# Performance work log

Measured on AMD Instinct MI355X. Metric: run time of the kernel, lower is better.

## Reference

```python
import jax, jax.numpy as jnp
import numpy as np

# dims
B, N, D, H, L = 2, 4096, 768, 12, 2
DH = D // H          # 64, equals BigBird block_size
BS = 64              # block size
NB = N // BS         # 64 blocks
R = 3                # num_random_blocks
FF = 4 * D
EPS = 1e-12          # BigBird layer_norm_eps


def _ln(x, g, b):
    mu = jnp.mean(x, -1, keepdims=True)
    var = jnp.mean(jnp.square(x - mu), -1, keepdims=True)
    return (x - mu) * jax.lax.rsqrt(var + EPS) * g + b


def _gelu_new(x):
    c = np.sqrt(2.0 / np.pi).astype(np.float32)
    return 0.5 * x * (1.0 + jnp.tanh(c * (x + 0.044715 * x * x * x)))


def _block_sparse_attn(q, k, v, rb):
    # q,k,v: [B,H,N,DH]; rb: [H,NB,R] random block ids (constant)
    scale = 1.0 / np.sqrt(DH).astype(np.float32)
    qb = q.reshape(B, H, NB, BS, DH)
    kb = k.reshape(B, H, NB, BS, DH)
    vb = v.reshape(B, H, NB, BS, DH)
    M = NB - 2
    mids = jnp.arange(1, NB - 1)
    win = jnp.stack([mids - 1, mids, mids + 1], -1)                    # [M,3]
    glb = jnp.broadcast_to(jnp.array([0, NB - 1], jnp.int32), (M, 2))  # [M,2]
    idx = jnp.concatenate([
        jnp.broadcast_to(glb[None], (H, M, 2)),
        jnp.broadcast_to(win[None], (H, M, 3)),
        rb[:, 1:NB - 1, :]], axis=-1)                                  # [H,M,8]
    hh = jnp.arange(H)[:, None, None]
    # gather key/value blocks: [B,H,M,8,BS,DH] -> [B,H,M,512,DH]
    kg = kb[:, hh, idx].reshape(B, H, M, -1, DH)
    vg = vb[:, hh, idx].reshape(B, H, M, -1, DH)
    qm = qb[:, :, 1:NB - 1]                                            # [B,H,M,BS,DH]
    s = jnp.einsum('bhmqd,bhmkd->bhmqk', qm, kg) * scale
    cm = jnp.einsum('bhmqk,bhmkd->bhmqd', jax.nn.softmax(s, -1), vg)
    # first and last query blocks attend globally (full attention)
    qe = jnp.stack([qb[:, :, 0], qb[:, :, -1]], 2)                     # [B,H,2,BS,DH]
    se = jnp.einsum('bheqd,bhkd->bheqk', qe, k) * scale
    ce = jnp.einsum('bheqk,bhkd->bheqd', jax.nn.softmax(se, -1), v)
    out = jnp.concatenate([ce[:, :, :1], cm, ce[:, :, 1:]], axis=2)    # [B,H,NB,BS,DH]
    return out.reshape(B, H, N, DH)


def _forward(inputs_embeds, rand_blocks, pos_emb, tt_emb, emb_ln_g, emb_ln_b,
             Wq, bq, Wk, bk, Wv, bv, Wo, bo, ln1_g, ln1_b,
             Wi, bi, Wd, bd, ln2_g, ln2_b, fc_w, fc_b):
    x = inputs_embeds + pos_emb[None] + tt_emb                         # embeddings (token_type id 0)
    x = _ln(x, emb_ln_g, emb_ln_b)
    for l in range(L):
        q = (x @ Wq[l] + bq[l]).reshape(B, N, H, DH).transpose(0, 2, 1, 3)
        k = (x @ Wk[l] + bk[l]).reshape(B, N, H, DH).transpose(0, 2, 1, 3)
        v = (x @ Wv[l] + bv[l]).reshape(B, N, H, DH).transpose(0, 2, 1, 3)
        ctx = _block_sparse_attn(q, k, v, rand_blocks[l])
        ctx = ctx.transpose(0, 2, 1, 3).reshape(B, N, D)
        a = _ln(x + ctx @ Wo[l] + bo[l], ln1_g[l], ln1_b[l])
        h = _gelu_new(a @ Wi[l] + bi[l])
        x = _ln(a + h @ Wd[l] + bd[l], ln2_g[l], ln2_b[l])
    pooled = jnp.mean(x, axis=1)                                       # [B,D]; dropout is identity at eval
    return (pooled @ fc_w + fc_b).squeeze()                            # [B]


def setup_inputs() -> dict:
    key = jax.random.key(0)
    ks = jax.random.split(key, 24)
    s = 0.02
    nrm = lambda k, shp: jax.random.normal(k, shp, jnp.float32) * s
    return {
        'inputs_embeds': jax.random.normal(ks[0], (B, N, D), jnp.float32),
        'rand_blocks': jax.random.randint(ks[1], (L, H, NB, R), 0, NB, jnp.int32),
        'pos_emb': nrm(ks[2], (N, D)),
        'tt_emb': nrm(ks[3], (D,)),
        'emb_ln_g': jnp.ones((D,), jnp.float32), 'emb_ln_b': jnp.zeros((D,), jnp.float32),
        'Wq': nrm(ks[4], (L, D, D)), 'bq': jnp.zeros((L, D), jnp.float32),
        'Wk': nrm(ks[5], (L, D, D)), 'bk': jnp.zeros((L, D), jnp.float32),
        'Wv': nrm(ks[6], (L, D, D)), 'bv': jnp.zeros((L, D), jnp.float32),
        'Wo': nrm(ks[7], (L, D, D)), 'bo': jnp.zeros((L, D), jnp.float32),
        'ln1_g': jnp.ones((L, D), jnp.float32), 'ln1_b': jnp.zeros((L, D), jnp.float32),
        'Wi': nrm(ks[8], (L, D, FF)), 'bi': jnp.zeros((L, FF), jnp.float32),
        'Wd': nrm(ks[9], (L, FF, D)), 'bd': jnp.zeros((L, D), jnp.float32),
        'ln2_g': jnp.ones((L, D), jnp.float32), 'ln2_b': jnp.zeros((L, D), jnp.float32),
        'fc_w': nrm(ks[10], (D, 1)), 'fc_b': jnp.zeros((1,), jnp.float32),
    }


def reference(inputs_embeds, rand_blocks, pos_emb, tt_emb, emb_ln_g, emb_ln_b,
              Wq, bq, Wk, bk, Wv, bv, Wo, bo, ln1_g, ln1_b,
              Wi, bi, Wd, bd, ln2_g, ln2_b, fc_w, fc_b):
    return _forward(inputs_embeds, rand_blocks, pos_emb, tt_emb, emb_ln_g, emb_ln_b,
                    Wq, bq, Wk, bk, Wv, bv, Wo, bo, ln1_g, ln1_b,
                    Wi, bi, Wd, bd, ln2_g, ln2_b, fc_w, fc_b)
```

## Files before the change

kernel.cpp:

```cpp
#include <hip/hip_runtime.h>
#include <math.h>

#define B_ 2
#define N_ 4096
#define D_ 768
#define H_ 12
#define DH_ 64
#define NB_ 64
#define FF_ 3072
#define LAYERS_ 2
#define ROWS_ (B_ * N_)

typedef __attribute__((ext_vector_type(8))) short s16x8;
typedef __attribute__((ext_vector_type(8))) unsigned short u16x8;
typedef __attribute__((ext_vector_type(4))) float f32x4;

typedef const __attribute__((address_space(1))) unsigned int ga_u32;
typedef __attribute__((address_space(3))) unsigned int lds_u32;

static __device__ __forceinline__ float gelu_fast(float x) {
    float z2 = 1.5957691216057308f * x * (1.0f + 0.044715f * x * x);
    return x * __builtin_amdgcn_rcpf(1.0f + __expf(-z2));
}

static __device__ __forceinline__ unsigned bf16_rne(float f) {
    unsigned u = __float_as_uint(f);
    return (u + 0x7FFFu + ((u >> 16) & 1u)) >> 16;
}
static __device__ __forceinline__ float bfh2f(unsigned short h) {
    return __uint_as_float(((unsigned)h) << 16);
}

__global__ __launch_bounds__(256)
void prep_weights(const float* __restrict__ Wq, const float* __restrict__ Wk,
                  const float* __restrict__ Wv, const float* __restrict__ Wo,
                  const float* __restrict__ Wi, const float* __restrict__ Wd,
                  unsigned short* __restrict__ Wt) {
    const size_t LW = 7077888;
    int bid = blockIdx.x;
    int l = bid / 1728, r = bid % 1728;
    const float* W; unsigned short* T; int K, N, t, nx;
    if (r < 576) {
        int which = r / 144; t = r % 144; nx = 12; K = 768; N = 768;
        W = (which == 0 ? Wq : which == 1 ? Wk : which == 2 ? Wv : Wo) + (size_t)l * D_ * D_;
        T = Wt + l * LW + (size_t)(which < 3 ? which * 768 * 768 : 2304 * 768);
    } else if (r < 1152) {
        t = r - 576; nx = 48; K = 768; N = 3072;
        W = Wi + (size_t)l * D_ * FF_;
        T = Wt + l * LW + (size_t)(2304 * 768 + 768 * 768);
    } else {
        t = r - 1152; nx = 12; K = 3072; N = 768;
        W = Wd + (size_t)l * FF_ * D_;
        T = Wt + l * LW + (size_t)(2304 * 768 + 768 * 768 + 3072 * 768);
    }
    const int bx = t % nx, by = t / nx;
    __shared__ unsigned short tile[64][72];
    const int k0 = by * 64, n0 = bx * 64;
    const int tt = threadIdx.x;
    const int rr = tt >> 2, c0 = (tt & 3) * 16;
    const float* src = W + (size_t)(k0 + rr) * N + n0 + c0;
#pragma unroll
    for (int j = 0; j < 4; ++j) {
        float4 v = *(const float4*)(src + j * 4);
        tile[rr][c0 + j * 4 + 0] = (unsigned short)bf16_rne(v.x);
        tile[rr][c0 + j * 4 + 1] = (unsigned short)bf16_rne(v.y);
        tile[rr][c0 + j * 4 + 2] = (unsigned short)bf16_rne(v.z);
        tile[rr][c0 + j * 4 + 3] = (unsigned short)bf16_rne(v.w);
    }
    __syncthreads();
    const int nr = tt >> 2, kc = (tt & 3) * 16;
    unsigned short* dst = T + (size_t)(n0 + nr) * K + k0 + kc;
    ushort4 o;
#pragma unroll
    for (int j = 0; j < 4; ++j) {
        o.x = tile[kc + j * 4 + 0][nr];
        o.y = tile[kc + j * 4 + 1][nr];
        o.z = tile[kc + j * 4 + 2][nr];
        o.w = tile[kc + j * 4 + 3][nr];
        *(ushort4*)(dst + j * 4) = o;
    }
}

template <int OMODE>
__global__ __launch_bounds__(256)
void gemm_bt(const unsigned short* __restrict__ A, const unsigned short* __restrict__ Bt,
             const float* __restrict__ bias, void* __restrict__ Cv,
             int N, int K, int gelu) {
    __shared__ __align__(16) unsigned short smem[2 * 8192];
    const int tid = threadIdx.x, lane = tid & 63, wid = tid >> 6;
    const int bid = blockIdx.x;
    const int row0 = (bid & 63) * 128, col0 = (bid >> 6) * 128;
    const int rh = (wid >> 1) * 64, ch = (wid & 1) * 64;
    const int fr = lane & 15, fq = lane >> 4;
    const int srow = wid * 32 + (lane >> 2);
    const int skoff = (lane & 3) * 8;
    const unsigned short* gA0 = A + (size_t)(row0 + srow) * K + skoff;
    const unsigned short* gA1 = gA0 + (size_t)16 * K;
    const unsigned short* gB0 = Bt + (size_t)(col0 + srow) * K + skoff;
    const unsigned short* gB1 = gB0 + (size_t)16 * K;

    f32x4 acc[4][4] = {};
    const int nk = K >> 5;

    {
        unsigned short* s = smem;
        __builtin_amdgcn_global_load_lds((ga_u32*)gA0, (lds_u32*)&s[wid * 1024], 16, 0, 0);
        __builtin_amdgcn_global_load_lds((ga_u32*)gA1, (lds_u32*)&s[wid * 1024 + 512], 16, 0, 0);
        __builtin_amdgcn_global_load_lds((ga_u32*)gB0, (lds_u32*)&s[4096 + wid * 1024], 16, 0, 0);
        __builtin_amdgcn_global_load_lds((ga_u32*)gB1, (lds_u32*)&s[4096 + wid * 1024 + 512], 16, 0, 0);
    }
    for (int kt = 0; kt < nk; ++kt) {
        __syncthreads();
        if (kt + 1 < nk) {
            int k0 = (kt + 1) << 5;
            unsigned short* s = smem + ((kt + 1) & 1) * 8192;
            __builtin_amdgcn_global_load_lds((ga_u32*)(gA0 + k0), (lds_u32*)&s[wid * 1024], 16, 0, 0);
            __builtin_amdgcn_global_load_lds((ga_u32*)(gA1 + k0), (lds_u32*)&s[wid * 1024 + 512], 16, 0, 0);
            __builtin_amdgcn_global_load_lds((ga_u32*)(gB0 + k0), (lds_u32*)&s[4096 + wid * 1024], 16, 0, 0);
            __builtin_amdgcn_global_load_lds((ga_u32*)(gB1 + k0), (lds_u32*)&s[4096 + wid * 1024 + 512], 16, 0, 0);
        }
        const unsigned short* sA = smem + (kt & 1) * 8192;
        const unsigned short* sB = sA + 4096;
        s16x8 af[4], bf[4];
#pragma unroll
        for (int i = 0; i < 4; ++i)
            af[i] = *(const s16x8*)&sA[(rh + 16 * i + fr) * 32 + fq * 8];
#pragma unroll
        for (int j = 0; j < 4; ++j)
            bf[j] = *(const s16x8*)&sB[(ch + 16 * j + fr) * 32 + fq * 8];
#pragma unroll
        for (int i = 0; i < 4; ++i)
#pragma unroll
            for (int j = 0; j < 4; ++j)
                acc[i][j] = __builtin_amdgcn_mfma_f32_16x16x32_bf16(af[i], bf[j], acc[i][j], 0, 0, 0);
    }
    if (OMODE == 0) {
#pragma unroll
        for (int j = 0; j < 4; ++j) {
            int col = col0 + ch + 16 * j + fr;
            float bb = bias[col];
#pragma unroll
            for (int i = 0; i < 4; ++i)
#pragma unroll
                for (int r = 0; r < 4; ++r) {
                    int row = row0 + rh + 16 * i + fq * 4 + r;
                    float v = acc[i][j][r] + bb;
                    if (gelu) v = gelu_fast(v);
                    ((float*)Cv)[(size_t)row * N + col] = v;
                }
        }
    } else {
        unsigned short* sC = smem;
#pragma unroll
        for (int hh = 0; hh < 2; ++hh) {
            __syncthreads();
            if ((wid >> 1) == hh) {
#pragma unroll
                for (int j = 0; j < 4; ++j) {
                    float bb = bias[col0 + ch + 16 * j + fr];
#pragma unroll
                    for (int i = 0; i < 4; ++i)
#pragma unroll
                        for (int r = 0; r < 4; ++r) {
                            float v = acc[i][j][r] + bb;
                            if (gelu) v = gelu_fast(v);
                            sC[(16 * i + fq * 4 + r) * 136 + ch + 16 * j + fr] =
                                (unsigned short)bf16_rne(v);
                        }
                }
            }
            __syncthreads();
#pragma unroll
            for (int p = 0; p < 4; ++p) {
                int seg = p * 256 + tid;
                int r = seg >> 4, c8 = (seg & 15) * 8;
                *(u16x8*)&((unsigned short*)Cv)[(size_t)(row0 + hh * 64 + r) * N + col0 + c8] =
                    *(const u16x8*)&sC[r * 136 + c8];
            }
        }
    }
}

__global__ __launch_bounds__(256)
void gemm_qkv(const unsigned short* __restrict__ A, const unsigned short* __restrict__ Bt,
              const float* __restrict__ bq, const float* __restrict__ bk,
              const float* __restrict__ bv,
              unsigned short* __restrict__ Qh, unsigned short* __restrict__ Kh,
              unsigned short* __restrict__ VT) {
    const int K = D_;
    __shared__ __align__(16) unsigned short smem[2 * 8192];
    const int tid = threadIdx.x, lane = tid & 63, wid = tid >> 6;
    const int bid = blockIdx.x;
    const int row0 = (bid & 63) * 128;
    const int bx = bid >> 6;
    const int col0 = bx * 128;
    const int rh = (wid >> 1) * 64, ch = (wid & 1) * 64;
    const int fr = lane & 15, fq = lane >> 4;
    const int srow = wid * 32 + (lane >> 2);
    const int skoff = (lane & 3) * 8;
    const unsigned short* gA0 = A + (size_t)(row0 + srow) * K + skoff;
    const unsigned short* gA1 = gA0 + (size_t)16 * K;
    const unsigned short* gB0 = Bt + (size_t)(col0 + srow) * K + skoff;
    const unsigned short* gB1 = gB0 + (size_t)16 * K;

    f32x4 acc[4][4] = {};
    const int nk = K >> 5;
    {
        unsigned short* s = smem;
        __builtin_amdgcn_global_load_lds((ga_u32*)gA0, (lds_u32*)&s[wid * 1024], 16, 0, 0);
        __builtin_amdgcn_global_load_lds((ga_u32*)gA1, (lds_u32*)&s[wid * 1024 + 512], 16, 0, 0);
        __builtin_amdgcn_global_load_lds((ga_u32*)gB0, (lds_u32*)&s[4096 + wid * 1024], 16, 0, 0);
        __builtin_amdgcn_global_load_lds((ga_u32*)gB1, (lds_u32*)&s[4096 + wid * 1024 + 512], 16, 0, 0);
    }
    for (int kt = 0; kt < nk; ++kt) {
        __syncthreads();
        if (kt + 1 < nk) {
            int k0 = (kt + 1) << 5;
            unsigned short* s = smem + ((kt + 1) & 1) * 8192;
            __builtin_amdgcn_global_load_lds((ga_u32*)(gA0 + k0), (lds_u32*)&s[wid * 1024], 16, 0, 0);
            __builtin_amdgcn_global_load_lds((ga_u32*)(gA1 + k0), (lds_u32*)&s[wid * 1024 + 512], 16, 0, 0);
            __builtin_amdgcn_global_load_lds((ga_u32*)(gB0 + k0), (lds_u32*)&s[4096 + wid * 1024], 16, 0, 0);
            __builtin_amdgcn_global_load_lds((ga_u32*)(gB1 + k0), (lds_u32*)&s[4096 + wid * 1024 + 512], 16, 0, 0);
        }
        const unsigned short* sA = smem + (kt & 1) * 8192;
        const unsigned short* sB = sA + 4096;
        s16x8 af[4], bf[4];
#pragma unroll
        for (int i = 0; i < 4; ++i)
            af[i] = *(const s16x8*)&sA[(rh + 16 * i + fr) * 32 + fq * 8];
#pragma unroll
        for (int j = 0; j < 4; ++j)
            bf[j] = *(const s16x8*)&sB[(ch + 16 * j + fr) * 32 + fq * 8];
#pragma unroll
        for (int i = 0; i < 4; ++i)
#pragma unroll
            for (int j = 0; j < 4; ++j)
                acc[i][j] = __builtin_amdgcn_mfma_f32_16x16x32_bf16(af[i], bf[j], acc[i][j], 0, 0, 0);
    }
    const int seg = bx / 6;
    const int colbase = col0 - seg * D_;
    const float* bias = (seg == 0) ? bq : (seg == 1) ? bk : bv;
    if (seg == 2) {
#pragma unroll
        for (int j = 0; j < 4; ++j) {
            int col_l = colbase + ch + 16 * j + fr;
            float bb = bias[col_l];
#pragma unroll
            for (int i = 0; i < 4; ++i) {
                int rowbase = row0 + rh + 16 * i + fq * 4;
                ushort4 o;
                o.x = (unsigned short)bf16_rne(acc[i][j][0] + bb);
                o.y = (unsigned short)bf16_rne(acc[i][j][1] + bb);
                o.z = (unsigned short)bf16_rne(acc[i][j][2] + bb);
                o.w = (unsigned short)bf16_rne(acc[i][j][3] + bb);
                *(ushort4*)&VT[(size_t)col_l * ROWS_ + rowbase] = o;
            }
        }
    } else {
        unsigned short* dst = (seg == 0) ? Qh : Kh;
        unsigned short* sC = smem;
#pragma unroll
        for (int hh = 0; hh < 2; ++hh) {
            __syncthreads();
            if ((wid >> 1) == hh) {
#pragma unroll
                for (int j = 0; j < 4; ++j) {
                    float bb = bias[colbase + ch + 16 * j + fr];
#pragma unroll
                    for (int i = 0; i < 4; ++i)
#pragma unroll
                        for (int r = 0; r < 4; ++r)
                            sC[(16 * i + fq * 4 + r) * 136 + ch + 16 * j + fr] =
                                (unsigned short)bf16_rne(acc[i][j][r] + bb);
                }
            }
            __syncthreads();
#pragma unroll
            for (int p = 0; p < 4; ++p) {
                int seg2 = p * 256 + tid;
                int r = seg2 >> 4, c8 = (seg2 & 15) * 8;
                *(u16x8*)&dst[(size_t)(row0 + hh * 64 + r) * D_ + colbase + c8] =
                    *(const u16x8*)&sC[r * 136 + c8];
            }
        }
    }
}

template <bool EDGE>
__global__ __launch_bounds__(256, 4)
void attn_mfma(const unsigned short* __restrict__ Qb, const unsigned short* __restrict__ Kb,
               const unsigned short* __restrict__ VTb, const int* __restrict__ rb,
               unsigned short* __restrict__ ctx, float* __restrict__ scratch) {
    __shared__ __align__(16) unsigned short sQ[64][72];
    __shared__ __align__(16) unsigned short sK[64][72];
    __shared__ __align__(16) unsigned short sVT[64][72];
    __shared__ __align__(16) unsigned short sP[4][16][72];
    __shared__ int sList[16];
    const int tid = threadIdx.x, lane = tid & 63, wid = tid >> 6;
    const int fr = lane & 15, fq = lane >> 4;
    int qb, h, b, nkb, slice = 0;
    if (EDGE) {
        int part = blockIdx.x & 3;
        int hh = (blockIdx.x >> 2) % H_;
        int be = (blockIdx.x >> 2) / H_;
        int eb = be & 1;
        b = be >> 1;
        h = hh;
        qb = eb ? (NB_ - 1) : 0;
        nkb = 16;
        slice = ((b * 2 + eb) * H_ + h) * 4 + part;
        if (tid < 16) sList[tid] = part * 16 + tid;
    } else {
        qb = blockIdx.x % (NB_ - 2) + 1;
        h = (blockIdx.x / (NB_ - 2)) % H_;
        b = blockIdx.x / ((NB_ - 2) * H_);
        nkb = 8;
        if (tid < 8) {
            int e;
            if (tid == 0) e = 0;
            else if (tid == 1) e = NB_ - 1;
            else if (tid < 5) e = qb + (tid - 3);
            else e = rb[(h * NB_ + qb) * 3 + (tid - 5)];
            sList[tid] = e;
        }
    }
    const int qrow0 = b * N_ + qb * 64;
    const unsigned short* Qg = Qb + (size_t)qrow0 * D_ + h * 64;
#pragma unroll
    for (int p = 0; p < 2; ++p) {
        int idx = p * 256 + tid;
        int r = idx >> 3, o = (idx & 7) * 8;
        *(u16x8*)&sQ[r][o] = *(const u16x8*)(Qg + (size_t)r * D_ + o);
    }
    f32x4 oacc[4] = {};
    float l_part[4] = {};
    __syncthreads();
    s16x8 aq0 = *(const s16x8*)&sQ[wid * 16 + fr][fq * 8];
    s16x8 aq1 = *(const s16x8*)&sQ[wid * 16 + fr][32 + fq * 8];

    for (int kb = 0; kb < nkb; ++kb) {
        const int kblk = sList[kb];
        const int keyrow0 = b * N_ + kblk * 64;
        __syncthreads();
        const unsigned short* Kg = Kb + (size_t)keyrow0 * D_ + h * 64;
#pragma unroll
        for (int p = 0; p < 2; ++p) {
            int idx = p * 256 + tid;
            int r = idx >> 3, o = (idx & 7) * 8;
            *(u16x8*)&sK[r][o] = *(const u16x8*)(Kg + (size_t)r * D_ + o);
        }
        const unsigned short* Vg = VTb + (size_t)(h * 64) * ROWS_ + keyrow0;
#pragma unroll
        for (int p = 0; p < 2; ++p) {
            int idx = p * 256 + tid;
            int d = idx >> 3, o = (idx & 7) * 8;
            *(u16x8*)&sVT[d][o] = *(const u16x8*)(Vg + (size_t)d * ROWS_ + o);
        }
        __syncthreads();
#pragma unroll
        for (int g = 0; g < 4; ++g) {
            s16x8 bk0 = *(const s16x8*)&sK[g * 16 + fr][fq * 8];
            s16x8 bk1 = *(const s16x8*)&sK[g * 16 + fr][32 + fq * 8];
            f32x4 s = {};
            s = __builtin_amdgcn_mfma_f32_16x16x32_bf16(aq0, bk0, s, 0, 0, 0);
            s = __builtin_amdgcn_mfma_f32_16x16x32_bf16(aq1, bk1, s, 0, 0, 0);
#pragma unroll
            for (int r = 0; r < 4; ++r) {
                float pv = __expf(s[r] * 0.125f);
                l_part[r] += pv;
                sP[wid][fq * 4 + r][g * 16 + fr] = (unsigned short)bf16_rne(pv);
            }
        }
        s16x8 ap0 = *(const s16x8*)&sP[wid][fr][fq * 8];
        s16x8 ap1 = *(const s16x8*)&sP[wid][fr][32 + fq * 8];
#pragma unroll
        for (int g = 0; g < 4; ++g) {
            s16x8 bv0 = *(const s16x8*)&sVT[g * 16 + fr][fq * 8];
            s16x8 bv1 = *(const s16x8*)&sVT[g * 16 + fr][32 + fq * 8];
            oacc[g] = __builtin_amdgcn_mfma_f32_16x16x32_bf16(ap0, bv0, oacc[g], 0, 0, 0);
            oacc[g] = __builtin_amdgcn_mfma_f32_16x16x32_bf16(ap1, bv1, oacc[g], 0, 0, 0);
        }
    }
    float l4[4];
#pragma unroll
    for (int r = 0; r < 4; ++r) {
        float lv = l_part[r];
        lv += __shfl_xor(lv, 1, 64);
        lv += __shfl_xor(lv, 2, 64);
        lv += __shfl_xor(lv, 4, 64);
        lv += __shfl_xor(lv, 8, 64);
        l4[r] = lv;
    }
    if (EDGE) {
        float* sc = scratch + (size_t)slice * (64 * 64 + 64);
#pragma unroll
        for (int g = 0; g < 4; ++g)
#pragma unroll
            for (int r = 0; r < 4; ++r)
                sc[(wid * 16 + fq * 4 + r) * 64 + g * 16 + fr] = oacc[g][r];
        if (fr == 0) {
#pragma unroll
            for (int r = 0; r < 4; ++r)
                sc[4096 + wid * 16 + fq * 4 + r] = l4[r];
        }
    } else {
        __syncthreads();
#pragma unroll
        for (int g = 0; g < 4; ++g) {
#pragma unroll
            for (int r = 0; r < 4; ++r) {
                float v = oacc[g][r] / l4[r];
                sK[wid * 16 + fq * 4 + r][g * 16 + fr] = (unsigned short)bf16_rne(v);
            }
        }
        __syncthreads();
        unsigned short* Cg = ctx + (size_t)qrow0 * D_ + h * 64;
#pragma unroll
        for (int p = 0; p < 2; ++p) {
            int idx = p * 256 + tid;
            int r = idx >> 3, o = (idx & 7) * 8;
            *(u16x8*)(Cg + (size_t)r * D_ + o) = *(const u16x8*)&sK[r][o];
        }
    }
}

__global__ __launch_bounds__(256)
void edge_combine(const float* __restrict__ scratch, unsigned short* __restrict__ ctx) {
    const int bid = blockIdx.x;
    const int h = bid % H_;
    const int eb = (bid / H_) & 1;
    const int b = bid / (2 * H_);
    const int qb = eb ? (NB_ - 1) : 0;
    const int qrow0 = b * N_ + qb * 64;
    const int slice0 = bid * 4;
    for (int e = threadIdx.x; e < 4096; e += 256) {
        int row = e >> 6, col = e & 63;
        float o = 0.f, l = 0.f;
#pragma unroll
        for (int p = 0; p < 4; ++p) {
            const float* sc = scratch + (size_t)(slice0 + p) * (64 * 64 + 64);
            o += sc[row * 64 + col];
            l += sc[4096 + row];
        }
        ctx[(size_t)(qrow0 + row) * D_ + h * 64 + col] = (unsigned short)bf16_rne(o / l);
    }
}

__global__ __launch_bounds__(256)
void embed_ln_kernel(const float* __restrict__ emb, const float* __restrict__ pos,
                     const float* __restrict__ tt, const float* __restrict__ g,
                     const float* __restrict__ bb, unsigned short* __restrict__ out) {
    __shared__ float red1[4], red2[4];
    const int row = blockIdx.x;
    const int n = row & (N_ - 1);
    const int t = threadIdx.x;
    float v[3];
#pragma unroll
    for (int i = 0; i < 3; ++i) {
        int d = t + i * 256;
        v[i] = emb[(size_t)row * D_ + d] + pos[(size_t)n * D_ + d] + tt[d];
    }
    float s = v[0] + v[1] + v[2];
#pragma unroll
    for (int off = 32; off > 0; off >>= 1) s += __shfl_xor(s, off, 64);
    if ((t & 63) == 0) red1[t >> 6] = s;
    __syncthreads();
    float mu = (red1[0] + red1[1] + red1[2] + red1[3]) * (1.0f / D_);
    float q = 0;
#pragma unroll
    for (int i = 0; i < 3; ++i) { float dv = v[i] - mu; q += dv * dv; }
#pragma unroll
    for (int off = 32; off > 0; off >>= 1) q += __shfl_xor(q, off, 64);
    if ((t & 63) == 0) red2[t >> 6] = q;
    __syncthreads();
    float var = (red2[0] + red2[1] + red2[2] + red2[3]) * (1.0f / D_);
    float rs = rsqrtf(var + 1e-12f);
#pragma unroll
    for (int i = 0; i < 3; ++i) {
        int d = t + i * 256;
        out[(size_t)row * D_ + d] = (unsigned short)bf16_rne((v[i] - mu) * rs * g[d] + bb[d]);
    }
}

__global__ __launch_bounds__(256)
void add_ln_kernel(const unsigned short* __restrict__ X, const float* __restrict__ Y,
                   const float* __restrict__ g, const float* __restrict__ bb,
                   unsigned short* __restrict__ out) {
    __shared__ float red1[4], red2[4];
    const int row = blockIdx.x;
    const int t = threadIdx.x;
    float v[3];
#pragma unroll
    for (int i = 0; i < 3; ++i) {
        int d = t + i * 256;
        v[i] = bfh2f(X[(size_t)row * D_ + d]) + Y[(size_t)row * D_ + d];
    }
    float s = v[0] + v[1] + v[2];
#pragma unroll
    for (int off = 32; off > 0; off >>= 1) s += __shfl_xor(s, off, 64);
    if ((t & 63) == 0) red1[t >> 6] = s;
    __syncthreads();
    float mu = (red1[0] + red1[1] + red1[2] + red1[3]) * (1.0f / D_);
    float q = 0;
#pragma unroll
    for (int i = 0; i < 3; ++i) { float dv = v[i] - mu; q += dv * dv; }
#pragma unroll
    for (int off = 32; off > 0; off >>= 1) q += __shfl_xor(q, off, 64);
    if ((t & 63) == 0) red2[t >> 6] = q;
    __syncthreads();
    float var = (red2[0] + red2[1] + red2[2] + red2[3]) * (1.0f / D_);
    float rs = rsqrtf(var + 1e-12f);
#pragma unroll
    for (int i = 0; i < 3; ++i) {
        int d = t + i * 256;
        out[(size_t)row * D_ + d] = (unsigned short)bf16_rne((v[i] - mu) * rs * g[d] + bb[d]);
    }
}

__global__ __launch_bounds__(256)
void pool_partial_kernel(const unsigned short* __restrict__ X, float* __restrict__ partial) {
    int blk = blockIdx.x;
    int b = blk >> 4, c = blk & 15;
    int t = threadIdx.x;
#pragma unroll
    for (int i = 0; i < 3; ++i) {
        int d = t + i * 256;
        float s = 0.f;
        for (int n = 0; n < 256; ++n)
            s += bfh2f(X[((size_t)(b * N_ + c * 256 + n)) * D_ + d]);
        partial[(size_t)(b * 16 + c) * D_ + d] = s;
    }
}

__global__ __launch_bounds__(256)
void pool_final_kernel(const float* __restrict__ partial, const float* __restrict__ fcw,
                       const float* __restrict__ fcb, float* __restrict__ out) {
    __shared__ float red[4];
    int t = threadIdx.x;
    for (int b = 0; b < B_; ++b) {
        float s = 0.f;
#pragma unroll
        for (int i = 0; i < 3; ++i) {
            int d = t + i * 256;
            float ps = 0.f;
#pragma unroll
            for (int c = 0; c < 16; ++c) ps += partial[(size_t)(b * 16 + c) * D_ + d];
            s += ps * (1.0f / N_) * fcw[d];
        }
#pragma unroll
        for (int off = 32; off > 0; off >>= 1) s += __shfl_xor(s, off, 64);
        __syncthreads();
        if ((t & 63) == 0) red[t >> 6] = s;
        __syncthreads();
        if (t == 0) out[b] = red[0] + red[1] + red[2] + red[3] + fcb[0];
    }
}

extern "C" void kernel_launch(void* const* d_in, const int* in_sizes, int n_in,
                              void* d_out, int out_size, void* d_ws, size_t ws_size,
                              hipStream_t stream) {
    (void)in_sizes; (void)n_in; (void)out_size; (void)ws_size;
    const float* emb  = (const float*)d_in[0];
    const int*   rblk = (const int*)d_in[1];
    const float* pos  = (const float*)d_in[2];
    const float* tt   = (const float*)d_in[3];
    const float* elg  = (const float*)d_in[4];
    const float* elb  = (const float*)d_in[5];
    const float* Wq   = (const float*)d_in[6];
    const float* bq   = (const float*)d_in[7];
    const float* Wk   = (const float*)d_in[8];
    const float* bk   = (const float*)d_in[9];
    const float* Wv   = (const float*)d_in[10];
    const float* bv   = (const float*)d_in[11];
    const float* Wo   = (const float*)d_in[12];
    const float* bo   = (const float*)d_in[13];
    const float* ln1g = (const float*)d_in[14];
    const float* ln1b = (const float*)d_in[15];
    const float* Wi   = (const float*)d_in[16];
    const float* bi   = (const float*)d_in[17];
    const float* Wd   = (const float*)d_in[18];
    const float* bd   = (const float*)d_in[19];
    const float* ln2g = (const float*)d_in[20];
    const float* ln2b = (const float*)d_in[21];
    const float* fcw  = (const float*)d_in[22];
    const float* fcb  = (const float*)d_in[23];
    float* outp = (float*)d_out;

    const size_t R = (size_t)ROWS_ * D_;
    float* base = (float*)d_ws;
    unsigned short* Xh  = (unsigned short*)base;
    unsigned short* Abh = (unsigned short*)(base + R / 2);
    float* G32 = base + R;
    unsigned short* Qh  = (unsigned short*)(base + 2 * R);
    unsigned short* Kh  = (unsigned short*)(base + 2 * R + R / 2);
    unsigned short* VTh = (unsigned short*)(base + 3 * R);
    unsigned short* Ch  = (unsigned short*)(base + 3 * R + R / 2);
    unsigned short* Hh  = (unsigned short*)(base + 2 * R);
    unsigned short* Wt  = (unsigned short*)(base + 4 * R);
    float* Esc = base + 4 * R + 7077888;
    float* Pp  = Esc + 798720;

    const size_t LW = 7077888;
    const int rows = ROWS_;
    dim3 blk(256);

    prep_weights<<<2 * 1728, blk, 0, stream>>>(Wq, Wk, Wv, Wo, Wi, Wd, Wt);

    embed_ln_kernel<<<rows, blk, 0, stream>>>(emb, pos, tt, elg, elb, Xh);

    for (int l = 0; l < LAYERS_; ++l) {
        const float* bq_l = bq + (size_t)l * D_;
        const float* bk_l = bk + (size_t)l * D_;
        const float* bv_l = bv + (size_t)l * D_;
        const float* bo_l = bo + (size_t)l * D_;
        const float* bi_l = bi + (size_t)l * FF_;
        const float* bd_l = bd + (size_t)l * D_;
        const float* l1g = ln1g + (size_t)l * D_;
        const float* l1b = ln1b + (size_t)l * D_;
        const float* l2g = ln2g + (size_t)l * D_;
        const float* l2b = ln2b + (size_t)l * D_;
        const int* rb_l = rblk + (size_t)l * H_ * NB_ * 3;
        unsigned short* QKVt = Wt + l * LW;
        unsigned short* Ot = QKVt + 2304 * 768;
        unsigned short* It = Ot + 768 * 768;
        unsigned short* Dt = It + 3072 * 768;

        gemm_qkv<<<18 * 64, blk, 0, stream>>>(Xh, QKVt, bq_l, bk_l, bv_l, Qh, Kh, VTh);

        attn_mfma<false><<<B_ * H_ * (NB_ - 2), blk, 0, stream>>>(Qh, Kh, VTh, rb_l, Ch, Esc);
        attn_mfma<true><<<B_ * 2 * H_ * 4, blk, 0, stream>>>(Qh, Kh, VTh, rb_l, Ch, Esc);
        edge_combine<<<B_ * 2 * H_, blk, 0, stream>>>(Esc, Ch);

        gemm_bt<0><<<6 * 64, blk, 0, stream>>>(Ch, Ot, bo_l, G32, D_, D_, 0);
        add_ln_kernel<<<rows, blk, 0, stream>>>(Xh, G32, l1g, l1b, Abh);

        gemm_bt<1><<<24 * 64, blk, 0, stream>>>(Abh, It, bi_l, Hh, FF_, D_, 1);
        gemm_bt<0><<<6 * 64, blk, 0, stream>>>(Hh, Dt, bd_l, G32, D_, FF_, 0);

        add_ln_kernel<<<rows, blk, 0, stream>>>(Abh, G32, l2g, l2b, Xh);
    }

    pool_partial_kernel<<<B_ * 16, blk, 0, stream>>>(Xh, Pp);
    pool_final_kernel<<<1, blk, 0, stream>>>(Pp, fcw, fcb, outp);
}
```

Baseline: 754.3 us.

## Prefetch K/V blocks into registers in attention; emit bf16 GEMM outputs for residual LN

The attention kernel now loads the next key/value block from global memory into registers while MFMA work runs on the current block held in LDS. This overlaps global load latency with compute at the cost of extra registers per thread. Separately, the output-projection and down-projection GEMMs now write bf16 instead of fp32. The add+LayerNorm kernels read that bf16 buffer, which halves the intermediate traffic but rounds the residual input to bf16 before normalisation.

```diff
diff --git a/kernel.cpp b/kernel.cpp
--- a/kernel.cpp
+++ b/kernel.cpp
@@ -101,7 +101,6 @@
 
     f32x4 acc[4][4] = {};
     const int nk = K >> 5;
-
     {
         unsigned short* s = smem;
         __builtin_amdgcn_global_load_lds((ga_u32*)gA0, (lds_u32*)&s[wid * 1024], 16, 0, 0);
@@ -338,25 +337,40 @@
     s16x8 aq0 = *(const s16x8*)&sQ[wid * 16 + fr][fq * 8];
     s16x8 aq1 = *(const s16x8*)&sQ[wid * 16 + fr][32 + fq * 8];
 
+    const int stg_r = tid >> 3, stg_o = (tid & 7) * 8;
+    u16x8 kreg[2], vreg[2];
+    {
+        int keyrow0 = b * N_ + sList[0] * 64;
+        const unsigned short* Kg = Kb + (size_t)keyrow0 * D_ + h * 64;
+        const unsigned short* Vg = VTb + (size_t)(h * 64) * ROWS_ + keyrow0;
+#pragma unroll
+        for (int p = 0; p < 2; ++p) {
+            int r = stg_r + p * 32;
+            kreg[p] = *(const u16x8*)(Kg + (size_t)r * D_ + stg_o);
+            vreg[p] = *(const u16x8*)(Vg + (size_t)r * ROWS_ + stg_o);
+        }
+    }
+
     for (int kb = 0; kb < nkb; ++kb) {
-        const int kblk = sList[kb];
-        const int keyrow0 = b * N_ + kblk * 64;
-        __syncthreads();
-        const unsigned short* Kg = Kb + (size_t)keyrow0 * D_ + h * 64;
+        __syncthreads();
 #pragma unroll
         for (int p = 0; p < 2; ++p) {
-            int idx = p * 256 + tid;
-            int r = idx >> 3, o = (idx & 7) * 8;
-            *(u16x8*)&sK[r][o] = *(const u16x8*)(Kg + (size_t)r * D_ + o);
-        }
-        const unsigned short* Vg = VTb + (size_t)(h * 64) * ROWS_ + keyrow0;
-#pragma unroll
-        for (int p = 0; p < 2; ++p) {
-            int idx = p * 256 + tid;
-            int d = idx >> 3, o = (idx & 7) * 8;
-            *(u16x8*)&sVT[d][o] = *(const u16x8*)(Vg + (size_t)d * ROWS_ + o);
-        }
-        __syncthreads();
+            int r = stg_r + p * 32;
+            *(u16x8*)&sK[r][stg_o] = kreg[p];
+            *(u16x8*)&sVT[r][stg_o] = vreg[p];
+        }
+        __syncthreads();
+        if (kb + 1 < nkb) {
+            int keyrow0 = b * N_ + sList[kb + 1] * 64;
+            const unsigned short* Kg = Kb + (size_t)keyrow0 * D_ + h * 64;
+            const unsigned short* Vg = VTb + (size_t)(h * 64) * ROWS_ + keyrow0;
+#pragma unroll
+            for (int p = 0; p < 2; ++p) {
+                int r = stg_r + p * 32;
+                kreg[p] = *(const u16x8*)(Kg + (size_t)r * D_ + stg_o);
+                vreg[p] = *(const u16x8*)(Vg + (size_t)r * ROWS_ + stg_o);
+            }
+        }
 #pragma unroll
         for (int g = 0; g < 4; ++g) {
             s16x8 bk0 = *(const s16x8*)&sK[g * 16 + fr][fq * 8];
@@ -483,7 +497,7 @@
 }
 
 __global__ __launch_bounds__(256)
-void add_ln_kernel(const unsigned short* __restrict__ X, const float* __restrict__ Y,
+void add_ln_kernel(const unsigned short* __restrict__ X, const unsigned short* __restrict__ Y,
                    const float* __restrict__ g, const float* __restrict__ bb,
                    unsigned short* __restrict__ out) {
     __shared__ float red1[4], red2[4];
@@ -493,7 +507,7 @@
 #pragma unroll
     for (int i = 0; i < 3; ++i) {
         int d = t + i * 256;
-        v[i] = bfh2f(X[(size_t)row * D_ + d]) + Y[(size_t)row * D_ + d];
+        v[i] = bfh2f(X[(size_t)row * D_ + d]) + bfh2f(Y[(size_t)row * D_ + d]);
     }
     float s = v[0] + v[1] + v[2];
 #pragma unroll
@@ -590,7 +604,7 @@
     float* base = (float*)d_ws;
     unsigned short* Xh  = (unsigned short*)base;
     unsigned short* Abh = (unsigned short*)(base + R / 2);
-    float* G32 = base + R;
+    unsigned short* Ob  = (unsigned short*)(base + R);
     unsigned short* Qh  = (unsigned short*)(base + 2 * R);
     unsigned short* Kh  = (unsigned short*)(base + 2 * R + R / 2);
     unsigned short* VTh = (unsigned short*)(base + 3 * R);
@@ -631,13 +645,13 @@
         attn_mfma<true><<<B_ * 2 * H_ * 4, blk, 0, stream>>>(Qh, Kh, VTh, rb_l, Ch, Esc);
         edge_combine<<<B_ * 2 * H_, blk, 0, stream>>>(Esc, Ch);
 
-        gemm_bt<0><<<6 * 64, blk, 0, stream>>>(Ch, Ot, bo_l, G32, D_, D_, 0);
-        add_ln_kernel<<<rows, blk, 0, stream>>>(Xh, G32, l1g, l1b, Abh);
+        gemm_bt<1><<<6 * 64, blk, 0, stream>>>(Ch, Ot, bo_l, Ob, D_, D_, 0);
+        add_ln_kernel<<<rows, blk, 0, stream>>>(Xh, Ob, l1g, l1b, Abh);
 
         gemm_bt<1><<<24 * 64, blk, 0, stream>>>(Abh, It, bi_l, Hh, FF_, D_, 1);
-        gemm_bt<0><<<6 * 64, blk, 0, stream>>>(Hh, Dt, bd_l, G32, D_, FF_, 0);
-
-        add_ln_kernel<<<rows, blk, 0, stream>>>(Abh, G32, l2g, l2b, Xh);
+        gemm_bt<1><<<6 * 64, blk, 0, stream>>>(Hh, Dt, bd_l, Ob, D_, FF_, 0);
+
+        add_ln_kernel<<<rows, blk, 0, stream>>>(Abh, Ob, l2g, l2b, Xh);
     }
 
     pool_partial_kernel<<<B_ * 16, blk, 0, stream>>>(Xh, Pp);
```

Measured after the change: 747.7 us. About the same (-0.9%).
